# Kernel optimization log

Hardware: AMD Instinct MI355X
Metric: run time of the kernel (lower is better)

## Reference

```python
import jax, jax.numpy as jnp
import numpy as np

B, N, E = 2, 10000, 160000
D, DC, L = 512, 8, 3
EPS = 1e-5


def layer_norm(x, g, b):
    m = jnp.mean(x, axis=-1, keepdims=True)
    v = jnp.mean((x - m) ** 2, axis=-1, keepdims=True)
    return (x - m) * jax.lax.rsqrt(v + EPS) * g + b


def setup_inputs() -> dict:
    key = jax.random.key(0)
    ks = jax.random.split(key, 8)
    node_features = jax.random.normal(ks[0], (B, N, D), dtype=jnp.float32)
    edge_index = jax.random.randint(ks[1], (2, E), 0, N, dtype=jnp.int64)
    edge_attr = jax.random.normal(ks[2], (E, D), dtype=jnp.float32)
    # manifold coordinate projection
    W_coord = jax.random.normal(ks[3], (D, DC), dtype=jnp.float32) / np.sqrt(D)
    # per-layer causal field layers (modeled as linear) and layer norms
    W_field = jax.random.normal(ks[4], (L, D, D), dtype=jnp.float32) / np.sqrt(D)
    b_field = jnp.zeros((L, D), dtype=jnp.float32)
    ln_g = jnp.ones((L, D), dtype=jnp.float32)
    ln_b = jnp.zeros((L, D), dtype=jnp.float32)
    # output projection: LayerNorm + Linear
    out_ln_g = jnp.ones((D,), dtype=jnp.float32)
    out_ln_b = jnp.zeros((D,), dtype=jnp.float32)
    W_out = jax.random.normal(ks[5], (D, D), dtype=jnp.float32) / np.sqrt(D)
    b_out = jnp.zeros((D,), dtype=jnp.float32)
    return dict(node_features=node_features, edge_index=edge_index, edge_attr=edge_attr,
                W_coord=W_coord, W_field=W_field, b_field=b_field, ln_g=ln_g, ln_b=ln_b,
                out_ln_g=out_ln_g, out_ln_b=out_ln_b, W_out=W_out, b_out=b_out)


def reference(node_features, edge_index, edge_attr, W_coord, W_field, b_field,
              ln_g, ln_b, out_ln_g, out_ln_b, W_out, b_out):
    src, dst = edge_index[0], edge_index[1]
    # node coordinates from manifold projection (computed once, from inputs)
    coords = node_features @ W_coord                        # (B, N, DC)
    # transport factor per edge, per batch: exp(-||dst_coord - src_coord||)
    coord_diff = coords[:, dst] - coords[:, src]            # (B, E, DC)
    transport = jnp.exp(-jnp.linalg.norm(coord_diff, axis=-1, keepdims=True))  # (B, E, 1)
    # degree of destination nodes (same for every batch element)
    deg = jnp.zeros((N,), dtype=node_features.dtype).at[dst].add(1.0)
    deg = jnp.clip(deg, 1.0, None)[None, :, None]           # (1, N, 1)

    x = node_features
    edge_msg = None
    for l in range(L):
        x_field = x @ W_field[l] + b_field[l]               # (B, N, D)
        # gather src features, apply transport, add edge attributes
        edge_msg = x_field[:, src] * transport + edge_attr[None]  # (B, E, D)
        # scatter-add into destination nodes, normalize by degree
        upd = jnp.zeros_like(x).at[:, dst].add(edge_msg)    # (B, N, D)
        x = layer_norm(x + upd / deg, ln_g[l], ln_b[l])
    node_output = layer_norm(x, out_ln_g, out_ln_b) @ W_out + b_out
    return node_output, edge_msg
```

## Files before the change

kernel.cpp:

```cpp
#include <hip/hip_runtime.h>
#include <stdint.h>

#define NN 10000
#define EE 160000
#define BB 2
#define DD 512
#define KC 1024
#define MVALID 20000
#define MPAD 20096
#define LEPS 1e-5f

typedef __bf16 bf16_t;
typedef __bf16 bf16x8 __attribute__((ext_vector_type(8)));
typedef float f32x4 __attribute__((ext_vector_type(4)));
typedef float f32x2 __attribute__((ext_vector_type(2)));

__device__ inline void gload16(const void* g, void* l) {
  __builtin_amdgcn_global_load_lds((const __attribute__((address_space(1))) uint32_t*)g,
                                   (__attribute__((address_space(3))) uint32_t*)l,
                                   16, 0, 0);
}

__global__ __launch_bounds__(256) void convw_k(const float* __restrict__ Wf,
                                               const float* __restrict__ Wo,
                                               const float* __restrict__ olng,
                                               bf16_t* __restrict__ wcat) {
  __shared__ float tile[64][65];
  const int kt = blockIdx.x, nt = blockIdx.y, l = blockIdx.z;
  const float* W = (l < 3) ? (Wf + (size_t)l * 262144) : Wo;
  const int tn = threadIdx.x & 63;
  const int tk = threadIdx.x >> 6;
#pragma unroll
  for (int i = 0; i < 16; i++) {
    const int kl = tk + i * 4;
    tile[kl][tn] = W[(size_t)(kt * 64 + kl) * 512 + nt * 64 + tn];
  }
  __syncthreads();
  const int kl2 = threadIdx.x & 63;
  const int nb = threadIdx.x >> 6;
  const float gk = (l == 3) ? olng[kt * 64 + kl2] : 1.0f;
#pragma unroll
  for (int i = 0; i < 16; i++) {
    const int nl = nb + i * 4;
    bf16_t h = (bf16_t)(tile[kl2][nl] * gk);
    wcat[((size_t)l * 512 + nt * 64 + nl) * 512 + kt * 64 + kl2] = h;
  }
}

__global__ __launch_bounds__(512) void ubinit_k(const float* __restrict__ bo, float* __restrict__ ub) {
  ub[threadIdx.x] = bo[threadIdx.x];
}
__global__ __launch_bounds__(256) void ubacc_k(const float* __restrict__ olnb,
                                               const float* __restrict__ Wo,
                                               float* __restrict__ ub) {
  const int k0 = blockIdx.x * 16;
  const int tid = threadIdx.x;
#pragma unroll
  for (int h = 0; h < 2; h++) {
    const int n = tid + h * 256;
    float s = 0.f;
#pragma unroll
    for (int kk = 0; kk < 16; kk++) s += olnb[k0 + kk] * Wo[(size_t)(k0 + kk) * 512 + n];
    atomicAdd(&ub[n], s);
  }
}

__global__ __launch_bounds__(256) void coords_k(const float* __restrict__ x,
                                                const float* __restrict__ Wc,
                                                float* __restrict__ out,
                                                bf16_t* __restrict__ xcat) {
  __shared__ float smW[DD * 8];
  for (int i = threadIdx.x; i < DD * 8; i += 256) smW[i] = Wc[i];
  __syncthreads();
  const int wave = threadIdx.x >> 6, lane = threadIdx.x & 63;
  const int n = blockIdx.x * 4 + wave;
  const int b = blockIdx.y;
  const size_t row = (size_t)b * NN + n;
  const float* xr = x + row * DD + lane * 8;
  f32x4 x0 = *(const f32x4*)xr;
  f32x4 x1 = *(const f32x4*)(xr + 4);
  bf16x8 hi, lo;
#pragma unroll
  for (int j = 0; j < 8; j++) {
    float v = (j < 4) ? x0[j] : x1[j - 4];
    bf16_t h = (bf16_t)v;
    hi[j] = h;
    lo[j] = (bf16_t)(v - (float)h);
  }
  bf16_t* xc = xcat + row * KC + lane * 8;
  *(bf16x8*)xc = hi;
  *(bf16x8*)(xc + DD) = lo;
  float a[8];
#pragma unroll
  for (int dc = 0; dc < 8; dc++) a[dc] = 0.f;
#pragma unroll
  for (int j = 0; j < 8; j++) {
    float xv = (j < 4) ? x0[j] : x1[j - 4];
    const float* wrow = smW + (lane * 8 + j) * 8;
#pragma unroll
    for (int dc = 0; dc < 8; dc++) a[dc] += xv * wrow[dc];
  }
#pragma unroll
  for (int dc = 0; dc < 8; dc++)
    for (int o = 32; o >= 1; o >>= 1) a[dc] += __shfl_xor(a[dc], o);
  if (lane == 0) {
#pragma unroll
    for (int dc = 0; dc < 8; dc++) out[row * 8 + dc] = a[dc];
  }
}

__global__ __launch_bounds__(256) void transport_deg_k(const float* __restrict__ coords,
                                                       const int* __restrict__ srcA,
                                                       const int* __restrict__ dstA,
                                                       float* __restrict__ tr,
                                                       int* __restrict__ degc) {
  int e = blockIdx.x * 256 + threadIdx.x;
  int s = srcA[e], d = dstA[e];
#pragma unroll
  for (int b = 0; b < BB; b++) {
    const float* cs = coords + ((size_t)b * NN + s) * 8;
    const float* cd = coords + ((size_t)b * NN + d) * 8;
    float ss = 0.f;
#pragma unroll
    for (int i = 0; i < 8; i++) {
      float df = cd[i] - cs[i];
      ss += df * df;
    }
    tr[(size_t)b * EE + e] = expf(-sqrtf(ss));
  }
  atomicAdd(&degc[d], 1);
}

__global__ __launch_bounds__(1024) void scan_k(const int* __restrict__ cnt, int* __restrict__ rowptr,
                                               float* __restrict__ invdeg) {
  __shared__ int part[1024];
  const int tid = threadIdx.x;
  const int CH = 10;
  int base = tid * CH;
  int local[CH];
  int s = 0;
#pragma unroll
  for (int i = 0; i < CH; i++) {
    int n = base + i;
    int c = (n < NN) ? cnt[n] : 0;
    local[i] = s;
    s += c;
  }
  part[tid] = s;
  __syncthreads();
  for (int off = 1; off < 1024; off <<= 1) {
    int v = (tid >= off) ? part[tid - off] : 0;
    __syncthreads();
    part[tid] += v;
    __syncthreads();
  }
  int excl = (tid > 0) ? part[tid - 1] : 0;
#pragma unroll
  for (int i = 0; i < CH; i++) {
    int n = base + i;
    if (n < NN) {
      rowptr[n] = excl + local[i];
      int c = cnt[n];
      invdeg[n] = 1.0f / (float)(c > 1 ? c : 1);
    }
  }
  if (tid == 0) rowptr[NN] = EE;
}

__global__ __launch_bounds__(256) void fillremap_k(const int* __restrict__ srcA,
                                                   const int* __restrict__ dstA,
                                                   const int* __restrict__ rowptr,
                                                   const float* __restrict__ tr,
                                                   const float* __restrict__ invdeg,
                                                   int* __restrict__ fill,
                                                   int* __restrict__ eidA,
                                                   int* __restrict__ srcs,
                                                   float* __restrict__ trs) {
  int e = blockIdx.x * 256 + threadIdx.x;
  const int d = dstA[e];
  const int pos = rowptr[d] + atomicAdd(&fill[d], 1);
  const float idg = invdeg[d];
  eidA[pos] = e;
  srcs[pos] = srcA[e];
  trs[pos] = tr[e] * idg;
  trs[(size_t)EE + pos] = tr[(size_t)EE + e] * idg;
}

__global__ __launch_bounds__(256) void gemm_bt_b(const bf16_t* __restrict__ A,
                                                 const bf16_t* __restrict__ Bw,
                                                 const float* __restrict__ bias,
                                                 bf16_t* __restrict__ C, int mvalid) {
  __shared__ __align__(16) char smem[16384];
  const int tid = threadIdx.x;
  const int lane = tid & 63;
  const int wave = tid >> 6;
  const int mtile = blockIdx.x;
  const int ntile = blockIdx.y;
  const int wr = wave >> 1, wc = wave & 1;
  const int r = tid >> 2;
  const int c = tid & 3;
  const size_t aRow0 = (size_t)(mtile * 128 + r);
  const size_t bRow0 = (size_t)(ntile * 128 + r);
  char* smA = smem;
  char* smB = smem + 8192;
  char* ldsA0 = smA + tid * 16;
  char* ldsA1 = smA + 4096 + tid * 16;
  char* ldsB0 = smB + tid * 16;
  char* ldsB1 = smB + 4096 + tid * 16;

  f32x4 acc[4][4];
#pragma unroll
  for (int m = 0; m < 4; m++)
#pragma unroll
    for (int n = 0; n < 4; n++) acc[m][n] = (f32x4){0.f, 0.f, 0.f, 0.f};

  const int koff = (lane >> 4) * 16;
  const int arow = wr * 64 + (lane & 15);
  const int brow = wc * 64 + (lane & 15);

  for (int kk = 0; kk < 16; ++kk) {
    const int kbase = kk * 32 + c * 8;
    gload16(A + aRow0 * KC + kbase, ldsA0);
    gload16(A + (aRow0 + 64) * KC + kbase, ldsA1);
    gload16(Bw + bRow0 * 512 + kbase, ldsB0);
    gload16(Bw + (bRow0 + 64) * 512 + kbase, ldsB1);
    __syncthreads();
    bf16x8 af[4], bfr[4];
#pragma unroll
    for (int m = 0; m < 4; m++) af[m] = *(const bf16x8*)(smA + (arow + m * 16) * 64 + koff);
#pragma unroll
    for (int n = 0; n < 4; n++) bfr[n] = *(const bf16x8*)(smB + (brow + n * 16) * 64 + koff);
#pragma unroll
    for (int m = 0; m < 4; m++)
#pragma unroll
      for (int n = 0; n < 4; n++)
        acc[m][n] = __builtin_amdgcn_mfma_f32_16x16x32_bf16(af[m], bfr[n], acc[m][n], 0, 0, 0);
    __syncthreads();
  }

  const int crow0 = mtile * 128 + wr * 64 + (lane >> 4) * 4;
  const int ccol0 = ntile * 128 + wc * 64 + (lane & 15);
#pragma unroll
  for (int n = 0; n < 4; n++) {
    const int col = ccol0 + n * 16;
    const float bv = bias[col];
#pragma unroll
    for (int m = 0; m < 4; m++) {
      const int rw = crow0 + m * 16;
#pragma unroll
      for (int j = 0; j < 4; j++) {
        int rowi = rw + j;
        if (rowi < mvalid) C[(size_t)rowi * DD + col] = (bf16_t)(acc[m][n][j] + bv);
      }
    }
  }
}

__global__ __launch_bounds__(256) void gemm_bt_f(const bf16_t* __restrict__ A,
                                                 const bf16_t* __restrict__ Bw,
                                                 const float* __restrict__ bias,
                                                 float* __restrict__ C, int mvalid,
                                                 const float* __restrict__ rs) {
  __shared__ __align__(16) char smem[16384];
  const int tid = threadIdx.x;
  const int lane = tid & 63;
  const int wave = tid >> 6;
  const int mtile = blockIdx.x;
  const int ntile = blockIdx.y;
  const int wr = wave >> 1, wc = wave & 1;
  const int r = tid >> 2;
  const int c = tid & 3;
  const size_t aRow0 = (size_t)(mtile * 128 + r);
  const size_t bRow0 = (size_t)(ntile * 128 + r);
  char* smA = smem;
  char* smB = smem + 8192;
  char* ldsA0 = smA + tid * 16;
  char* ldsA1 = smA + 4096 + tid * 16;
  char* ldsB0 = smB + tid * 16;
  char* ldsB1 = smB + 4096 + tid * 16;

  f32x4 acc[4][4];
#pragma unroll
  for (int m = 0; m < 4; m++)
#pragma unroll
    for (int n = 0; n < 4; n++) acc[m][n] = (f32x4){0.f, 0.f, 0.f, 0.f};

  const int koff = (lane >> 4) * 16;
  const int arow = wr * 64 + (lane & 15);
  const int brow = wc * 64 + (lane & 15);

  for (int kk = 0; kk < 16; ++kk) {
    const int kbase = kk * 32 + c * 8;
    gload16(A + aRow0 * KC + kbase, ldsA0);
    gload16(A + (aRow0 + 64) * KC + kbase, ldsA1);
    gload16(Bw + bRow0 * 512 + kbase, ldsB0);
    gload16(Bw + (bRow0 + 64) * 512 + kbase, ldsB1);
    __syncthreads();
    bf16x8 af[4], bfr[4];
#pragma unroll
    for (int m = 0; m < 4; m++) af[m] = *(const bf16x8*)(smA + (arow + m * 16) * 64 + koff);
#pragma unroll
    for (int n = 0; n < 4; n++) bfr[n] = *(const bf16x8*)(smB + (brow + n * 16) * 64 + koff);
#pragma unroll
    for (int m = 0; m < 4; m++)
#pragma unroll
      for (int n = 0; n < 4; n++)
        acc[m][n] = __builtin_amdgcn_mfma_f32_16x16x32_bf16(af[m], bfr[n], acc[m][n], 0, 0, 0);
    __syncthreads();
  }

  const int crow0 = mtile * 128 + wr * 64 + (lane >> 4) * 4;
  const int ccol0 = ntile * 128 + wc * 64 + (lane & 15);
#pragma unroll
  for (int n = 0; n < 4; n++) {
    const int col = ccol0 + n * 16;
    const float bv = bias[col];
#pragma unroll
    for (int m = 0; m < 4; m++) {
      const int rw = crow0 + m * 16;
#pragma unroll
      for (int j = 0; j < 4; j++) {
        int rowi = rw + j;
        if (rowi < mvalid) C[(size_t)rowi * DD + col] = acc[m][n][j] * rs[rowi] + bv;
      }
    }
  }
}

template <int FUSE_EA>
__device__ inline void layer_body(int n, int lane,
                                  const bf16_t* __restrict__ xfield, int outstat,
                                  bf16_t* __restrict__ xcat,
                                  const int* __restrict__ srcs,
                                  const float* __restrict__ trs,
                                  const int* __restrict__ rowptr,
                                  const int* __restrict__ eidA,
                                  const float* __restrict__ eattr,
                                  const float* __restrict__ invdeg,
                                  float* __restrict__ eagg,
                                  const float* __restrict__ g,
                                  const float* __restrict__ bbias,
                                  float* __restrict__ rs_out) {
  const int d0 = lane * 8;
  const int beg = rowptr[n], end = rowptr[n + 1];
  const bf16_t* xf0 = xfield + (size_t)0 * NN * DD + d0;
  const bf16_t* xf1 = xfield + (size_t)1 * NN * DD + d0;
  const float* trs1p = trs + EE;
  float acc0[8], acc1[8], eac[8];
#pragma unroll
  for (int j = 0; j < 8; j++) acc0[j] = acc1[j] = eac[j] = 0.f;

  for (int c0 = beg; c0 < end; c0 += 64) {
    const int cnt = min(64, end - c0);
    int s_r = 0, e_r = 0;
    float t0_r = 0.f, t1_r = 0.f;
    if (lane < cnt) {
      s_r = srcs[c0 + lane];
      t0_r = trs[c0 + lane];
      t1_r = trs1p[c0 + lane];
      if (FUSE_EA) e_r = eidA[c0 + lane];
    }
    for (int j = 0; j < cnt; j += 4) {
#pragma unroll
      for (int u = 0; u < 4; u++) {
        const int jj = j + u;
        const int s = __shfl(s_r, jj);
        const float t0 = __shfl(t0_r, jj);
        const float t1 = __shfl(t1_r, jj);
        const bf16x8 xv0 = *(const bf16x8*)(xf0 + (size_t)s * DD);
        const bf16x8 xv1 = *(const bf16x8*)(xf1 + (size_t)s * DD);
        if (FUSE_EA) {
          const int e = __shfl(e_r, jj);
          const bool act = jj < cnt;
          const f32x4 r0 = __builtin_nontemporal_load((const f32x4*)(eattr + (size_t)e * DD + d0));
          const f32x4 r1 = __builtin_nontemporal_load((const f32x4*)(eattr + (size_t)e * DD + d0 + 4));
          if (act) {
#pragma unroll
            for (int q = 0; q < 8; q++) eac[q] += (q < 4) ? r0[q & 3] : r1[q & 3];
          }
        }
#pragma unroll
        for (int q = 0; q < 8; q++) {
          acc0[q] += t0 * (float)xv0[q];
          acc1[q] += t1 * (float)xv1[q];
        }
      }
    }
  }

  float ea8[8];
  if (FUSE_EA) {
    const float idg = invdeg[n];
#pragma unroll
    for (int j = 0; j < 8; j++) ea8[j] = eac[j] * idg;
    f32x4 o0, o1;
#pragma unroll
    for (int j = 0; j < 4; j++) {
      o0[j] = ea8[j];
      o1[j] = ea8[j + 4];
    }
    *(f32x4*)(eagg + (size_t)n * DD + d0) = o0;
    *(f32x4*)(eagg + (size_t)n * DD + d0 + 4) = o1;
  } else {
    const f32x4 e0 = *(const f32x4*)(eagg + (size_t)n * DD + d0);
    const f32x4 e1 = *(const f32x4*)(eagg + (size_t)n * DD + d0 + 4);
#pragma unroll
    for (int j = 0; j < 8; j++) ea8[j] = (j < 4) ? e0[j] : e1[j - 4];
  }

  bf16_t* xc0 = xcat + (size_t)n * KC + d0;
  bf16_t* xc1 = xcat + (size_t)(NN + n) * KC + d0;
  const bf16x8 h0 = *(const bf16x8*)(xc0);
  const bf16x8 l0v = *(const bf16x8*)(xc0 + DD);
  const bf16x8 h1 = *(const bf16x8*)(xc1);
  const bf16x8 l1v = *(const bf16x8*)(xc1 + DD);
  float v0[8], v1[8];
  float s10 = 0.f, s20 = 0.f, s11 = 0.f, s21 = 0.f;
#pragma unroll
  for (int j = 0; j < 8; j++) {
    const float xp0 = (float)h0[j] + (float)l0v[j];
    const float xp1 = (float)h1[j] + (float)l1v[j];
    v0[j] = xp0 + acc0[j] + ea8[j];
    v1[j] = xp1 + acc1[j] + ea8[j];
    s10 += v0[j];
    s20 += v0[j] * v0[j];
    s11 += v1[j];
    s21 += v1[j] * v1[j];
  }
#pragma unroll
  for (int o = 32; o >= 1; o >>= 1) {
    s10 += __shfl_xor(s10, o);
    s20 += __shfl_xor(s20, o);
    s11 += __shfl_xor(s11, o);
    s21 += __shfl_xor(s21, o);
  }
  const float mean0 = s10 * (1.f / 512.f);
  const float rs0 = rsqrtf(s20 * (1.f / 512.f) - mean0 * mean0 + LEPS);
  const float mean1 = s11 * (1.f / 512.f);
  const float rs1 = rsqrtf(s21 * (1.f / 512.f) - mean1 * mean1 + LEPS);
  const f32x4 g0 = *(const f32x4*)(g + d0);
  const f32x4 g1 = *(const f32x4*)(g + d0 + 4);
  const f32x4 b0 = *(const f32x4*)(bbias + d0);
  const f32x4 b1 = *(const f32x4*)(bbias + d0 + 4);
  float y0[8], y1[8];
  float sy10 = 0.f, sy20 = 0.f, sy11 = 0.f, sy21 = 0.f;
#pragma unroll
  for (int j = 0; j < 8; j++) {
    const float gg = (j < 4) ? g0[j] : g1[j - 4];
    const float bb = (j < 4) ? b0[j] : b1[j - 4];
    y0[j] = (v0[j] - mean0) * rs0 * gg + bb;
    y1[j] = (v1[j] - mean1) * rs1 * gg + bb;
    sy10 += y0[j];
    sy20 += y0[j] * y0[j];
    sy11 += y1[j];
    sy21 += y1[j] * y1[j];
  }
  float sub0 = 0.f, sub1 = 0.f;
  if (outstat) {
#pragma unroll
    for (int o = 32; o >= 1; o >>= 1) {
      sy10 += __shfl_xor(sy10, o);
      sy20 += __shfl_xor(sy20, o);
      sy11 += __shfl_xor(sy11, o);
      sy21 += __shfl_xor(sy21, o);
    }
    const float my0 = sy10 * (1.f / 512.f);
    const float rsy0 = rsqrtf(sy20 * (1.f / 512.f) - my0 * my0 + LEPS);
    const float my1 = sy11 * (1.f / 512.f);
    const float rsy1 = rsqrtf(sy21 * (1.f / 512.f) - my1 * my1 + LEPS);
    if (lane == 0) {
      rs_out[n] = rsy0;
      rs_out[NN + n] = rsy1;
    }
    sub0 = my0;
    sub1 = my1;
  }
  bf16x8 ho0, lo0, ho1, lo1;
#pragma unroll
  for (int j = 0; j < 8; j++) {
    const float ya = y0[j] - sub0;
    const float yb = y1[j] - sub1;
    bf16_t ha = (bf16_t)ya;
    bf16_t hb = (bf16_t)yb;
    ho0[j] = ha;
    lo0[j] = (bf16_t)(ya - (float)ha);
    ho1[j] = hb;
    lo1[j] = (bf16_t)(yb - (float)hb);
  }
  *(bf16x8*)xc0 = ho0;
  *(bf16x8*)xc1 = ho1;
  if (!outstat) {
    *(bf16x8*)(xc0 + DD) = lo0;
    *(bf16x8*)(xc1 + DD) = lo1;
  }
}

template <int FUSE_EA>
__global__ __launch_bounds__(256) void layer_k(const bf16_t* __restrict__ xfield,
                                               bf16_t* __restrict__ xcat,
                                               const int* __restrict__ srcs,
                                               const float* __restrict__ trs,
                                               const int* __restrict__ rowptr,
                                               const int* __restrict__ eidA,
                                               const float* __restrict__ eattr,
                                               const float* __restrict__ invdeg,
                                               float* __restrict__ eagg,
                                               const float* __restrict__ g,
                                               const float* __restrict__ bbias) {
  const int wave = threadIdx.x >> 6, lane = threadIdx.x & 63;
  const int n = blockIdx.x * 4 + wave;
  layer_body<FUSE_EA>(n, lane, xfield, 0, xcat, srcs, trs, rowptr, eidA, eattr, invdeg, eagg, g,
                      bbias, nullptr);
}

__global__ __launch_bounds__(256) void tail_k(const bf16_t* __restrict__ xfield,
                                              bf16_t* __restrict__ xcat,
                                              const int* __restrict__ srcs,
                                              const float* __restrict__ trs,
                                              const int* __restrict__ rowptr,
                                              const float* __restrict__ eagg,
                                              const float* __restrict__ g,
                                              const float* __restrict__ bbias,
                                              float* __restrict__ rs_out,
                                              const float* __restrict__ transport,
                                              const int* __restrict__ srcA,
                                              const float* __restrict__ eattr,
                                              float* __restrict__ outE) {
  const int bid = blockIdx.x;
  const int wv = threadIdx.x >> 6, lane = threadIdx.x & 63;
  if (bid < 2500) {
    const int n = bid * 4 + wv;
    layer_body<0>(n, lane, xfield, 1, xcat, srcs, trs, rowptr, nullptr, nullptr, nullptr,
                  (float*)eagg, g, bbias, rs_out);
  } else {
    const int e = (bid - 2500) * 4 + wv;
    const int d0 = lane * 8;
    const int s = srcA[e];
    const f32x4 a0 = __builtin_nontemporal_load((const f32x4*)(eattr + (size_t)e * DD + d0));
    const f32x4 a1 = __builtin_nontemporal_load((const f32x4*)(eattr + (size_t)e * DD + d0 + 4));
    const float t0 = transport[e];
    const float t1 = transport[(size_t)EE + e];
    const bf16x8 x0 = *(const bf16x8*)(xfield + (size_t)s * DD + d0);
    const bf16x8 x1 = *(const bf16x8*)(xfield + ((size_t)NN + s) * DD + d0);
    f32x4 o00, o01, o10, o11;
#pragma unroll
    for (int j = 0; j < 4; j++) {
      o00[j] = (float)x0[j] * t0 + a0[j];
      o01[j] = (float)x0[j + 4] * t0 + a1[j];
      o10[j] = (float)x1[j] * t1 + a0[j];
      o11[j] = (float)x1[j + 4] * t1 + a1[j];
    }
    float* ob0 = outE + (size_t)e * DD + d0;
    float* ob1 = outE + ((size_t)EE + e) * DD + d0;
    __builtin_nontemporal_store(o00, (f32x4*)ob0);
    __builtin_nontemporal_store(o01, (f32x4*)(ob0 + 4));
    __builtin_nontemporal_store(o10, (f32x4*)ob1);
    __builtin_nontemporal_store(o11, (f32x4*)(ob1 + 4));
  }
}

extern "C" void kernel_launch(void* const* d_in, const int* in_sizes, int n_in,
                              void* d_out, int out_size, void* d_ws, size_t ws_size,
                              hipStream_t stream) {
  const float* nf = (const float*)d_in[0];
  const int* eidx = (const int*)d_in[1];
  const float* eattr = (const float*)d_in[2];
  const float* Wc = (const float*)d_in[3];
  const float* Wf = (const float*)d_in[4];
  const float* bfield = (const float*)d_in[5];
  const float* lng = (const float*)d_in[6];
  const float* lnb = (const float*)d_in[7];
  const float* olng = (const float*)d_in[8];
  const float* olnb = (const float*)d_in[9];
  const float* Wo = (const float*)d_in[10];
  const float* bo = (const float*)d_in[11];
  const int* srcA = eidx;
  const int* dstA = eidx + EE;
  float* outp = (float*)d_out;

  char* ws = (char*)d_ws;
  size_t off = 0;
  auto alloc = [&](size_t bytes) {
    void* p = ws + off;
    off += (bytes + 255) & ~(size_t)255;
    return p;
  };
  bf16_t* xcat = (bf16_t*)alloc((size_t)MPAD * KC * 2);
  bf16_t* xfield = (bf16_t*)alloc((size_t)MPAD * DD * 2);
  bf16_t* wcat = (bf16_t*)alloc((size_t)4 * DD * 512 * 2);
  float* eagg = (float*)alloc((size_t)NN * DD * 4);
  float* coords = (float*)alloc((size_t)BB * NN * 8 * 4);
  float* transport = (float*)alloc((size_t)BB * EE * 4);
  float* trs = (float*)alloc((size_t)BB * EE * 4);
  int* srcs = (int*)alloc(EE * 4);
  int* degfill = (int*)alloc((size_t)2 * NN * 4);
  int* degc = degfill;
  int* fillb = degfill + NN;
  int* rowptr = (int*)alloc((NN + 1) * 4);
  int* eidl = (int*)alloc(EE * 4);
  float* invdeg = (float*)alloc(NN * 4);
  float* rs_out = (float*)alloc((size_t)BB * NN * 4);
  float* ub = (float*)alloc(DD * 4);

  hipMemsetAsync(degfill, 0, (size_t)2 * NN * 4, stream);
  hipMemsetAsync(xcat + (size_t)MVALID * KC, 0, (size_t)(MPAD - MVALID) * KC * 2, stream);

  convw_k<<<dim3(8, 8, 4), 256, 0, stream>>>(Wf, Wo, olng, wcat);
  ubinit_k<<<1, 512, 0, stream>>>(bo, ub);
  ubacc_k<<<32, 256, 0, stream>>>(olnb, Wo, ub);
  coords_k<<<dim3(2500, 2), 256, 0, stream>>>(nf, Wc, coords, xcat);
  transport_deg_k<<<625, 256, 0, stream>>>(coords, srcA, dstA, transport, degc);
  scan_k<<<1, 1024, 0, stream>>>(degc, rowptr, invdeg);
  fillremap_k<<<625, 256, 0, stream>>>(srcA, dstA, rowptr, transport, invdeg, fillb, eidl, srcs,
                                       trs);

  for (int l = 0; l < 2; l++) {
    gemm_bt_b<<<dim3(157, 4), 256, 0, stream>>>(xcat, wcat + (size_t)l * DD * 512,
                                                bfield + l * DD, xfield, MVALID);
    if (l == 0)
      layer_k<1><<<2500, 256, 0, stream>>>(xfield, xcat, srcs, trs, rowptr, eidl, eattr, invdeg,
                                           eagg, lng + l * DD, lnb + l * DD);
    else
      layer_k<0><<<2500, 256, 0, stream>>>(xfield, xcat, srcs, trs, rowptr, eidl, eattr, invdeg,
                                           eagg, lng + l * DD, lnb + l * DD);
  }
  gemm_bt_b<<<dim3(157, 4), 256, 0, stream>>>(xcat, wcat + (size_t)2 * DD * 512, bfield + 2 * DD,
                                              xfield, MVALID);
  tail_k<<<42500, 256, 0, stream>>>(xfield, xcat, srcs, trs, rowptr, eagg, lng + 2 * DD,
                                    lnb + 2 * DD, rs_out, transport, srcA, eattr,
                                    outp + (size_t)BB * NN * DD);
  gemm_bt_f<<<dim3(157, 4), 256, 0, stream>>>(xcat, wcat + (size_t)3 * DD * 512, ub, outp, MVALID,
                                              rs_out);
}
```

Before: 644.8 us.

## Split node aggregation across batch elements, one wave per (node, batch)

```diff
diff --git a/kernel.cpp b/kernel.cpp
--- a/kernel.cpp
+++ b/kernel.cpp
@@ -13,7 +13,6 @@
 typedef __bf16 bf16_t;
 typedef __bf16 bf16x8 __attribute__((ext_vector_type(8)));
 typedef float f32x4 __attribute__((ext_vector_type(4)));
-typedef float f32x2 __attribute__((ext_vector_type(2)));
 
 __device__ inline void gload16(const void* g, void* l) {
   __builtin_amdgcn_global_load_lds((const __attribute__((address_space(1))) uint32_t*)g,
@@ -328,7 +327,7 @@
 }
 
 template <int FUSE_EA>
-__device__ inline void layer_body(int n, int lane,
+__device__ inline void layer_body(int n, int b, int lane,
                                   const bf16_t* __restrict__ xfield, int outstat,
                                   bf16_t* __restrict__ xcat,
                                   const int* __restrict__ srcs,
@@ -343,21 +342,21 @@
                                   float* __restrict__ rs_out) {
   const int d0 = lane * 8;
   const int beg = rowptr[n], end = rowptr[n + 1];
-  const bf16_t* xf0 = xfield + (size_t)0 * NN * DD + d0;
-  const bf16_t* xf1 = xfield + (size_t)1 * NN * DD + d0;
-  const float* trs1p = trs + EE;
-  float acc0[8], acc1[8], eac[8];
-#pragma unroll
-  for (int j = 0; j < 8; j++) acc0[j] = acc1[j] = eac[j] = 0.f;
+  const bf16_t* xf = xfield + (size_t)b * NN * DD + d0;
+  const float* trsb = trs + (size_t)b * EE;
+  const int eoff = d0 + b * 4;
+  float acc[8];
+  f32x4 eac4 = (f32x4){0.f, 0.f, 0.f, 0.f};
+#pragma unroll
+  for (int j = 0; j < 8; j++) acc[j] = 0.f;
 
   for (int c0 = beg; c0 < end; c0 += 64) {
     const int cnt = min(64, end - c0);
     int s_r = 0, e_r = 0;
-    float t0_r = 0.f, t1_r = 0.f;
+    float t_r = 0.f;
     if (lane < cnt) {
       s_r = srcs[c0 + lane];
-      t0_r = trs[c0 + lane];
-      t1_r = trs1p[c0 + lane];
+      t_r = trsb[c0 + lane];
       if (FUSE_EA) e_r = eidA[c0 + lane];
     }
     for (int j = 0; j < cnt; j += 4) {
@@ -365,134 +364,88 @@
       for (int u = 0; u < 4; u++) {
         const int jj = j + u;
         const int s = __shfl(s_r, jj);
-        const float t0 = __shfl(t0_r, jj);
-        const float t1 = __shfl(t1_r, jj);
-        const bf16x8 xv0 = *(const bf16x8*)(xf0 + (size_t)s * DD);
-        const bf16x8 xv1 = *(const bf16x8*)(xf1 + (size_t)s * DD);
+        const float t = __shfl(t_r, jj);
+        const bf16x8 xv = *(const bf16x8*)(xf + (size_t)s * DD);
         if (FUSE_EA) {
           const int e = __shfl(e_r, jj);
-          const bool act = jj < cnt;
-          const f32x4 r0 = __builtin_nontemporal_load((const f32x4*)(eattr + (size_t)e * DD + d0));
-          const f32x4 r1 = __builtin_nontemporal_load((const f32x4*)(eattr + (size_t)e * DD + d0 + 4));
-          if (act) {
-#pragma unroll
-            for (int q = 0; q < 8; q++) eac[q] += (q < 4) ? r0[q & 3] : r1[q & 3];
+          const f32x4 r = __builtin_nontemporal_load((const f32x4*)(eattr + (size_t)e * DD + eoff));
+          if (jj < cnt) {
+#pragma unroll
+            for (int q = 0; q < 4; q++) eac4[q] += r[q];
           }
         }
 #pragma unroll
-        for (int q = 0; q < 8; q++) {
-          acc0[q] += t0 * (float)xv0[q];
-          acc1[q] += t1 * (float)xv1[q];
-        }
+        for (int q = 0; q < 8; q++) acc[q] += t * (float)xv[q];
       }
     }
   }
 
-  float ea8[8];
   if (FUSE_EA) {
     const float idg = invdeg[n];
-#pragma unroll
-    for (int j = 0; j < 8; j++) ea8[j] = eac[j] * idg;
-    f32x4 o0, o1;
-#pragma unroll
-    for (int j = 0; j < 4; j++) {
-      o0[j] = ea8[j];
-      o1[j] = ea8[j + 4];
-    }
-    *(f32x4*)(eagg + (size_t)n * DD + d0) = o0;
-    *(f32x4*)(eagg + (size_t)n * DD + d0 + 4) = o1;
-  } else {
-    const f32x4 e0 = *(const f32x4*)(eagg + (size_t)n * DD + d0);
-    const f32x4 e1 = *(const f32x4*)(eagg + (size_t)n * DD + d0 + 4);
-#pragma unroll
-    for (int j = 0; j < 8; j++) ea8[j] = (j < 4) ? e0[j] : e1[j - 4];
-  }
-
-  bf16_t* xc0 = xcat + (size_t)n * KC + d0;
-  bf16_t* xc1 = xcat + (size_t)(NN + n) * KC + d0;
-  const bf16x8 h0 = *(const bf16x8*)(xc0);
-  const bf16x8 l0v = *(const bf16x8*)(xc0 + DD);
-  const bf16x8 h1 = *(const bf16x8*)(xc1);
-  const bf16x8 l1v = *(const bf16x8*)(xc1 + DD);
-  float v0[8], v1[8];
-  float s10 = 0.f, s20 = 0.f, s11 = 0.f, s21 = 0.f;
+    f32x4 o;
+#pragma unroll
+    for (int q = 0; q < 4; q++) o[q] = eac4[q] * idg;
+    *(f32x4*)(eagg + (size_t)n * DD + eoff) = o;
+    __syncthreads();
+  }
+  const f32x4 e0 = *(const f32x4*)(eagg + (size_t)n * DD + d0);
+  const f32x4 e1 = *(const f32x4*)(eagg + (size_t)n * DD + d0 + 4);
+
+  bf16_t* xc = xcat + ((size_t)b * NN + n) * KC + d0;
+  const bf16x8 h = *(const bf16x8*)(xc);
+  const bf16x8 lv = *(const bf16x8*)(xc + DD);
+  float v[8];
+  float s1 = 0.f, s2 = 0.f;
 #pragma unroll
   for (int j = 0; j < 8; j++) {
-    const float xp0 = (float)h0[j] + (float)l0v[j];
-    const float xp1 = (float)h1[j] + (float)l1v[j];
-    v0[j] = xp0 + acc0[j] + ea8[j];
-    v1[j] = xp1 + acc1[j] + ea8[j];
-    s10 += v0[j];
-    s20 += v0[j] * v0[j];
-    s11 += v1[j];
-    s21 += v1[j] * v1[j];
+    const float ea = (j < 4) ? e0[j] : e1[j - 4];
+    v[j] = (float)h[j] + (float)lv[j] + acc[j] + ea;
+    s1 += v[j];
+    s2 += v[j] * v[j];
   }
 #pragma unroll
   for (int o = 32; o >= 1; o >>= 1) {
-    s10 += __shfl_xor(s10, o);
-    s20 += __shfl_xor(s20, o);
-    s11 += __shfl_xor(s11, o);
-    s21 += __shfl_xor(s21, o);
-  }
-  const float mean0 = s10 * (1.f / 512.f);
-  const float rs0 = rsqrtf(s20 * (1.f / 512.f) - mean0 * mean0 + LEPS);
-  const float mean1 = s11 * (1.f / 512.f);
-  const float rs1 = rsqrtf(s21 * (1.f / 512.f) - mean1 * mean1 + LEPS);
+    s1 += __shfl_xor(s1, o);
+    s2 += __shfl_xor(s2, o);
+  }
+  const float mean = s1 * (1.f / 512.f);
+  const float rsv = rsqrtf(s2 * (1.f / 512.f) - mean * mean + LEPS);
   const f32x4 g0 = *(const f32x4*)(g + d0);
   const f32x4 g1 = *(const f32x4*)(g + d0 + 4);
   const f32x4 b0 = *(const f32x4*)(bbias + d0);
   const f32x4 b1 = *(const f32x4*)(bbias + d0 + 4);
-  float y0[8], y1[8];
-  float sy10 = 0.f, sy20 = 0.f, sy11 = 0.f, sy21 = 0.f;
+  float y[8];
+  float sy1 = 0.f, sy2 = 0.f;
 #pragma unroll
   for (int j = 0; j < 8; j++) {
     const float gg = (j < 4) ? g0[j] : g1[j - 4];
     const float bb = (j < 4) ? b0[j] : b1[j - 4];
-    y0[j] = (v0[j] - mean0) * rs0 * gg + bb;
-    y1[j] = (v1[j] - mean1) * rs1 * gg + bb;
-    sy10 += y0[j];
-    sy20 += y0[j] * y0[j];
-    sy11 += y1[j];
-    sy21 += y1[j] * y1[j];
-  }
-  float sub0 = 0.f, sub1 = 0.f;
+    y[j] = (v[j] - mean) * rsv * gg + bb;
+    sy1 += y[j];
+    sy2 += y[j] * y[j];
+  }
+  float sub = 0.f;
   if (outstat) {
 #pragma unroll
     for (int o = 32; o >= 1; o >>= 1) {
-      sy10 += __shfl_xor(sy10, o);
-      sy20 += __shfl_xor(sy20, o);
-      sy11 += __shfl_xor(sy11, o);
-      sy21 += __shfl_xor(sy21, o);
-    }
-    const float my0 = sy10 * (1.f / 512.f);
-    const float rsy0 = rsqrtf(sy20 * (1.f / 512.f) - my0 * my0 + LEPS);
-    const float my1 = sy11 * (1.f / 512.f);
-    const float rsy1 = rsqrtf(sy21 * (1.f / 512.f) - my1 * my1 + LEPS);
-    if (lane == 0) {
-      rs_out[n] = rsy0;
-      rs_out[NN + n] = rsy1;
-    }
-    sub0 = my0;
-    sub1 = my1;
-  }
-  bf16x8 ho0, lo0, ho1, lo1;
+      sy1 += __shfl_xor(sy1, o);
+      sy2 += __shfl_xor(sy2, o);
+    }
+    const float my = sy1 * (1.f / 512.f);
+    const float rsy = rsqrtf(sy2 * (1.f / 512.f) - my * my + LEPS);
+    if (lane == 0) rs_out[(size_t)b * NN + n] = rsy;
+    sub = my;
+  }
+  bf16x8 ho, lo;
 #pragma unroll
   for (int j = 0; j < 8; j++) {
-    const float ya = y0[j] - sub0;
-    const float yb = y1[j] - sub1;
+    const float ya = y[j] - sub;
     bf16_t ha = (bf16_t)ya;
-    bf16_t hb = (bf16_t)yb;
-    ho0[j] = ha;
-    lo0[j] = (bf16_t)(ya - (float)ha);
-    ho1[j] = hb;
-    lo1[j] = (bf16_t)(yb - (float)hb);
-  }
-  *(bf16x8*)xc0 = ho0;
-  *(bf16x8*)xc1 = ho1;
-  if (!outstat) {
-    *(bf16x8*)(xc0 + DD) = lo0;
-    *(bf16x8*)(xc1 + DD) = lo1;
-  }
+    ho[j] = ha;
+    lo[j] = (bf16_t)(ya - (float)ha);
+  }
+  *(bf16x8*)xc = ho;
+  if (!outstat) *(bf16x8*)(xc + DD) = lo;
 }
 
 template <int FUSE_EA>
@@ -508,9 +461,10 @@
                                                const float* __restrict__ g,
                                                const float* __restrict__ bbias) {
   const int wave = threadIdx.x >> 6, lane = threadIdx.x & 63;
-  const int n = blockIdx.x * 4 + wave;
-  layer_body<FUSE_EA>(n, lane, xfield, 0, xcat, srcs, trs, rowptr, eidA, eattr, invdeg, eagg, g,
-                      bbias, nullptr);
+  const int slot = blockIdx.x * 4 + wave;
+  const int n = slot >> 1, b = slot & 1;
+  layer_body<FUSE_EA>(n, b, lane, xfield, 0, xcat, srcs, trs, rowptr, eidA, eattr, invdeg, eagg,
+                      g, bbias, nullptr);
 }
 
 __global__ __launch_bounds__(256) void tail_k(const bf16_t* __restrict__ xfield,
@@ -528,12 +482,13 @@
                                               float* __restrict__ outE) {
   const int bid = blockIdx.x;
   const int wv = threadIdx.x >> 6, lane = threadIdx.x & 63;
-  if (bid < 2500) {
-    const int n = bid * 4 + wv;
-    layer_body<0>(n, lane, xfield, 1, xcat, srcs, trs, rowptr, nullptr, nullptr, nullptr,
+  if (bid < 5000) {
+    const int slot = bid * 4 + wv;
+    const int n = slot >> 1, b = slot & 1;
+    layer_body<0>(n, b, lane, xfield, 1, xcat, srcs, trs, rowptr, nullptr, nullptr, nullptr,
                   (float*)eagg, g, bbias, rs_out);
   } else {
-    const int e = (bid - 2500) * 4 + wv;
+    const int e = (bid - 5000) * 4 + wv;
     const int d0 = lane * 8;
     const int s = srcA[e];
     const f32x4 a0 = __builtin_nontemporal_load((const f32x4*)(eattr + (size_t)e * DD + d0));
@@ -618,15 +573,15 @@
     gemm_bt_b<<<dim3(157, 4), 256, 0, stream>>>(xcat, wcat + (size_t)l * DD * 512,
                                                 bfield + l * DD, xfield, MVALID);
     if (l == 0)
-      layer_k<1><<<2500, 256, 0, stream>>>(xfield, xcat, srcs, trs, rowptr, eidl, eattr, invdeg,
-                                           eagg, lng + l * DD, lnb + l * DD);
+      layer_k<1><<<5000, 256, 0, stream>>>(xfield, xcat, srcs, trs, rowptr, eidl, eattr, invdeg,
+                                           eagg, lng, lnb);
     else
-      layer_k<0><<<2500, 256, 0, stream>>>(xfield, xcat, srcs, trs, rowptr, eidl, eattr, invdeg,
-                                           eagg, lng + l * DD, lnb + l * DD);
+      layer_k<0><<<5000, 256, 0, stream>>>(xfield, xcat, srcs, trs, rowptr, eidl, eattr, invdeg,
+                                           eagg, lng + DD, lnb + DD);
   }
   gemm_bt_b<<<dim3(157, 4), 256, 0, stream>>>(xcat, wcat + (size_t)2 * DD * 512, bfield + 2 * DD,
                                               xfield, MVALID);
-  tail_k<<<42500, 256, 0, stream>>>(xfield, xcat, srcs, trs, rowptr, eagg, lng + 2 * DD,
+  tail_k<<<45000, 256, 0, stream>>>(xfield, xcat, srcs, trs, rowptr, eagg, lng + 2 * DD,
                                     lnb + 2 * DD, rs_out, transport, srcA, eattr,
                                     outp + (size_t)BB * NN * DD);
   gemm_bt_f<<<dim3(157, 4), 256, 0, stream>>>(xcat, wcat + (size_t)3 * DD * 512, ub, outp, MVALID,
```

New measurement: 656.4 us. Within noise of the previous version (+1.8%).
